# Kernel tuning notes

Hardware: AMD Instinct MI355X
Metric: run time of the kernel (lower is better)

The kernel has to match this reference:

```python
import jax, jax.numpy as jnp
import numpy as np

B, T, FEATS, HEAD = 2, 2048, 2048, 16
DIM_HEAD = FEATS // HEAD
EPS = float(jnp.finfo(jnp.float32).eps)  # torch nn.RMSNorm default eps=None -> dtype eps


def _rms_norm(u, g):
    # u: [..., d]; torch RMSNorm: u / sqrt(mean(u^2) + eps) * g
    return u * jax.lax.rsqrt(jnp.mean(u * u, axis=-1, keepdims=True) + EPS) * g


def setup_inputs() -> dict:
    key = jax.random.key(0)
    kx, kw = jax.random.split(key)
    x = jax.random.normal(kx, (B, T, FEATS), dtype=jnp.float32)
    W = jax.random.normal(kw, (FEATS, FEATS), dtype=jnp.float32) / np.sqrt(FEATS)
    g1 = jnp.ones((DIM_HEAD,), dtype=jnp.float32)
    g2 = jnp.ones((DIM_HEAD,), dtype=jnp.float32)
    g3 = jnp.ones((DIM_HEAD,), dtype=jnp.float32)
    return {"x": x, "W": W, "g1": g1, "g2": g2, "g3": g3}


def reference(x, W, g1, g2, g3):
    Bb, Tt, C = x.shape
    sqrt_d = jnp.asarray(DIM_HEAD ** 0.5, dtype=x.dtype)
    # tied QKV projection: torch Linear -> x @ W.T ; then split heads -> [B,H,T,D]
    w = (x @ W.T).reshape(Bb, Tt, HEAD, DIM_HEAD).transpose(0, 2, 1, 3)
    q = _rms_norm(w, g1)
    k = _rms_norm(w, g2)
    v = _rms_norm(w, g3)
    att = jnp.einsum("bhid,bhjd->bhij", q, k) / sqrt_d  # [B,H,T,T]
    # symmetric row + column softmax
    score = jax.nn.softmax(att, axis=-1) + jax.nn.softmax(att, axis=-2)
    y = jnp.einsum("bhij,bhjd->bihd", score, v).reshape(Bb, Tt, C)
    # F.linear(y, W.t()) == y @ W  (tied-weight reprojection)
    return y @ W
```

## Files before the change

### kernel.cpp

```cpp
#include <hip/hip_runtime.h>
#include <stdint.h>

#define T_SEQ 2048
#define B_SZ 2
#define N_HEAD 16
#define D_HEAD 128
#define C_DIM 2048
#define M_ROWS (B_SZ*T_SEQ)
#define N_BH (B_SZ*N_HEAD)

typedef _Float16 f16;
typedef f16 f16x8 __attribute__((ext_vector_type(8)));
typedef f16 f16x4 __attribute__((ext_vector_type(4)));
typedef float f32x4 __attribute__((ext_vector_type(4)));

#define MFMA_F16(a,b,c) __builtin_amdgcn_mfma_f32_16x16x32_f16(a,b,c,0,0,0)

#define BAR_LGKM() do { asm volatile("s_waitcnt lgkmcnt(0)" ::: "memory"); \
                        __builtin_amdgcn_s_barrier(); } while (0)
#define BAR_ALL()  do { asm volatile("s_waitcnt vmcnt(0) lgkmcnt(0)" ::: "memory"); \
                        __builtin_amdgcn_s_barrier(); } while (0)

__device__ __forceinline__ float fexp2(float x) {
#if __has_builtin(__builtin_amdgcn_exp2f)
  return __builtin_amdgcn_exp2f(x);
#else
  float r; asm("v_exp_f32 %0, %1" : "=v"(r) : "v"(x)); return r;
#endif
}

__device__ __forceinline__ void gl_lds16(const void* g, void* l) {
  __builtin_amdgcn_global_load_lds(
      (const __attribute__((address_space(1))) unsigned int*)g,
      (__attribute__((address_space(3))) unsigned int*)l, 16, 0, 0);
}

#define MB_SCALE 0.12752924444069595f
#define RMS_EPS  1.1920928955078125e-07f

__global__ void k_prep(const float* __restrict__ W, const float* __restrict__ x,
                       f16* __restrict__ Wb, f16* __restrict__ Wtb,
                       f16* __restrict__ xb) {
  __shared__ float tile[64][65];
  const int lin = blockIdx.x;
  const int t = threadIdx.x;
  if (lin < 1024) {
    const int bx = (lin & 31) * 64;
    const int by = (lin >> 5) * 64;
    const int tc = t & 63, tr4 = t >> 6;
    for (int rr = tr4; rr < 64; rr += 4) {
      float v = W[(size_t)(by + rr) * C_DIM + bx + tc];
      tile[rr][tc] = v;
      Wb[(size_t)(by + rr) * C_DIM + bx + tc] = (f16)v;
    }
    __syncthreads();
    for (int rr = tr4; rr < 64; rr += 4) {
      Wtb[(size_t)(bx + rr) * C_DIM + by + tc] = (f16)tile[tc][rr];
    }
  } else {
    int i = (lin - 1024) * 256 + t;
    const int stride = 2048 * 256;
    const int n4 = (M_ROWS * C_DIM) / 4;
    for (; i < n4; i += stride) {
      f32x4 v = ((const f32x4*)x)[i];
      f16x4 o; o[0]=(f16)v[0]; o[1]=(f16)v[1]; o[2]=(f16)v[2]; o[3]=(f16)v[3];
      ((f16x4*)xb)[i] = o;
    }
  }
}

template<typename OT>
__global__ __launch_bounds__(256, 2)
void k_gemm_bt(const f16* __restrict__ A, const f16* __restrict__ Bm,
               OT* __restrict__ C, int Nd, int Kd) {
  __shared__ __align__(16) f16 As[2][128 * 64];
  __shared__ __align__(16) f16 Bs[2][128 * 64];
  const int tid = threadIdx.x;
  const int lane = tid & 63, wid = tid >> 6;
  const int lr = lane & 15, lkg = lane >> 4;
  const int wr = wid >> 1, wc = wid & 1;
  const int tm = blockIdx.y * 128, tn = blockIdx.x * 128;

  f32x4 acc[4][4];
#pragma unroll
  for (int i = 0; i < 4; ++i)
#pragma unroll
    for (int j = 0; j < 4; ++j) acc[i][j] = (f32x4){0.f, 0.f, 0.f, 0.f};

  const int nkt = Kd >> 6;

  auto stage = [&](int buf, int kt) {
    const int k0 = kt << 6;
    for (int s = 0; s < 4; ++s) {
      const int r0 = (wid * 4 + s) * 8;
      const int r = r0 + (lane >> 3);
      const int lg = ((lane & 7) ^ (r & 7)) << 3;
      gl_lds16(A + (size_t)(tm + r) * Kd + k0 + lg, &As[buf][r0 * 64]);
      gl_lds16(Bm + (size_t)(tn + r) * Kd + k0 + lg, &Bs[buf][r0 * 64]);
    }
  };

  stage(0, 0);
  int cur = 0;
  for (int kt = 0; kt < nkt; ++kt) {
    __syncthreads();
    if (kt + 1 < nkt) stage(cur ^ 1, kt + 1);
#pragma unroll
    for (int kk = 0; kk < 2; ++kk) {
      f16x8 a[4], b[4];
#pragma unroll
      for (int i = 0; i < 4; ++i) {
        const int ra = wr * 64 + i * 16 + lr;
        const int ga = ((kk * 4 + lkg) ^ (ra & 7)) << 3;
        a[i] = *(const f16x8*)&As[cur][ra * 64 + ga];
        const int rb = wc * 64 + i * 16 + lr;
        const int gb = ((kk * 4 + lkg) ^ (rb & 7)) << 3;
        b[i] = *(const f16x8*)&Bs[cur][rb * 64 + gb];
      }
#pragma unroll
      for (int i = 0; i < 4; ++i)
#pragma unroll
        for (int j = 0; j < 4; ++j) acc[i][j] = MFMA_F16(a[i], b[j], acc[i][j]);
    }
    cur ^= 1;
  }
#pragma unroll
  for (int i = 0; i < 4; ++i) {
    const int row0 = tm + wr * 64 + i * 16 + lkg * 4;
#pragma unroll
    for (int j = 0; j < 4; ++j) {
      const int col = tn + wc * 64 + j * 16 + lr;
#pragma unroll
      for (int r = 0; r < 4; ++r)
        C[(size_t)(row0 + r) * Nd + col] = (OT)acc[i][j][r];
    }
  }
}

__global__ __launch_bounds__(256, 2)
void k_gemm_qkv(const f16* __restrict__ A, const f16* __restrict__ Bm,
                const float* __restrict__ g1, const float* __restrict__ g2,
                f16* __restrict__ nb, f16* __restrict__ mb,
                f16* __restrict__ nT) {
  __shared__ __align__(16) char smem[70656];
  f16 (*As)[128 * 64] = (f16(*)[128 * 64])smem;
  f16 (*Bs)[128 * 64] = (f16(*)[128 * 64])(smem + 32768);
  f16* Cs = (f16*)smem;
  float* sc = (float*)(smem + 69632);

  const int tid = threadIdx.x;
  const int lane = tid & 63, wid = tid >> 6;
  const int lr = lane & 15, lkg = lane >> 4;
  const int wr = wid >> 1, wc = wid & 1;
  const int tm = blockIdx.y * 128;
  const int hh = blockIdx.x;
  const int tn = hh * 128;

  f32x4 acc[4][4];
#pragma unroll
  for (int i = 0; i < 4; ++i)
#pragma unroll
    for (int j = 0; j < 4; ++j) acc[i][j] = (f32x4){0.f, 0.f, 0.f, 0.f};

  auto stage = [&](int buf, int kt) {
    const int k0 = kt << 6;
    for (int s = 0; s < 4; ++s) {
      const int r0 = (wid * 4 + s) * 8;
      const int r = r0 + (lane >> 3);
      const int lg = ((lane & 7) ^ (r & 7)) << 3;
      gl_lds16(A + (size_t)(tm + r) * C_DIM + k0 + lg, &As[buf][r0 * 64]);
      gl_lds16(Bm + (size_t)(tn + r) * C_DIM + k0 + lg, &Bs[buf][r0 * 64]);
    }
  };

  stage(0, 0);
  int cur = 0;
  for (int kt = 0; kt < 32; ++kt) {
    __syncthreads();
    if (kt + 1 < 32) stage(cur ^ 1, kt + 1);
#pragma unroll
    for (int kk = 0; kk < 2; ++kk) {
      f16x8 a[4], b[4];
#pragma unroll
      for (int i = 0; i < 4; ++i) {
        const int ra = wr * 64 + i * 16 + lr;
        const int ga = ((kk * 4 + lkg) ^ (ra & 7)) << 3;
        a[i] = *(const f16x8*)&As[cur][ra * 64 + ga];
        const int rb = wc * 64 + i * 16 + lr;
        const int gb = ((kk * 4 + lkg) ^ (rb & 7)) << 3;
        b[i] = *(const f16x8*)&Bs[cur][rb * 64 + gb];
      }
#pragma unroll
      for (int i = 0; i < 4; ++i)
#pragma unroll
        for (int j = 0; j < 4; ++j) acc[i][j] = MFMA_F16(a[i], b[j], acc[i][j]);
    }
    cur ^= 1;
  }
  __syncthreads();

#pragma unroll
  for (int i = 0; i < 4; ++i)
#pragma unroll
    for (int j = 0; j < 4; ++j)
#pragma unroll
      for (int r = 0; r < 4; ++r)
        Cs[(wr * 64 + i * 16 + lkg * 4 + r) * 136 + wc * 64 + j * 16 + lr] =
            (f16)acc[i][j][r];
  __syncthreads();

  const int row = tid >> 1, dh = tid & 1;
  f16x8 v[8];
  float ss = 0.f;
#pragma unroll
  for (int c = 0; c < 8; ++c) {
    v[c] = *(const f16x8*)&Cs[row * 136 + dh * 64 + c * 8];
#pragma unroll
    for (int e = 0; e < 8; ++e) { float f = (float)v[c][e]; ss += f * f; }
  }
  ss += __shfl_xor(ss, 1);
  const float scale = rsqrtf(ss * (1.f / 128.f) + RMS_EPS);
  if (dh == 0) sc[row] = scale;

  const int grow = tm + row;
  const int b = grow >> 11, ts = grow & (T_SEQ - 1);
  const size_t nbase =
      ((size_t)((b * N_HEAD + hh) * T_SEQ + ts)) * 128 + dh * 64;
#pragma unroll
  for (int c = 0; c < 8; ++c) {
    const int d0 = dh * 64 + c * 8;
    f16x8 n8, m8;
#pragma unroll
    for (int e = 0; e < 8; ++e) {
      const float nf = (float)v[c][e] * scale;
      n8[e] = (f16)nf;
      m8[e] = (f16)(nf * g1[d0 + e] * g2[d0 + e] * MB_SCALE);
    }
    *(f16x8*)&nb[nbase + c * 8] = n8;
    *(f16x8*)&mb[nbase + c * 8] = m8;
  }
  __syncthreads();

  const int dcol = tid >> 1, th = tid & 1;
  const size_t tbase =
      ((size_t)((b * N_HEAD + hh) * 128 + dcol)) * T_SEQ + (tm & (T_SEQ - 1)) +
      th * 64;
#pragma unroll
  for (int rr = 0; rr < 8; ++rr) {
    f16x8 o;
#pragma unroll
    for (int e = 0; e < 8; ++e) {
      const int trow = th * 64 + rr * 8 + e;
      o[e] = (f16)((float)Cs[trow * 136 + dcol] * sc[trow]);
    }
    *(f16x8*)&nT[tbase + rr * 8] = o;
  }
}

__global__ __launch_bounds__(256, 2)
void k_stats(const f16* __restrict__ mIn, const f16* __restrict__ nIn,
             float* __restrict__ alpha) {
  __shared__ __align__(16) f16 Ns[2][128 * 128];
  __shared__ float red[256];
  const int tid = threadIdx.x, lane = tid & 63, wid = tid >> 6;
  const int lr = lane & 15, lkg = lane >> 4;
  const int wr = wid >> 1, wc = wid & 1;
  const int lin = blockIdx.x + (blockIdx.y << 4);
  const int swz = ((lin & 7) << 6) + (lin >> 3);
  const int it = swz & 15, bh = swz >> 4;
  const f16* mp = mIn + (size_t)bh * T_SEQ * 128;
  const f16* np = nIn + (size_t)bh * T_SEQ * 128;

  f16x8 msr[4][4];
#pragma unroll
  for (int i = 0; i < 4; ++i)
#pragma unroll
    for (int kk = 0; kk < 4; ++kk)
      msr[i][kk] = *(const f16x8*)&mp[(size_t)(it * 128 + wr * 64 + i * 16 + lr) * 128 +
                                      (kk * 4 + lkg) * 8];

  auto stageN = [&](int buf, int jt) {
#pragma unroll
    for (int s = 0; s < 8; ++s) {
      const int r0 = (wid * 8 + s) * 4;
      const int r = r0 + (lane >> 4);
      const int lg = ((lane & 15) ^ (r & 7)) << 3;
      gl_lds16(np + (size_t)(jt * 128 + r) * 128 + lg, &Ns[buf][r0 * 128]);
    }
  };

  float srun[16];
#pragma unroll
  for (int q = 0; q < 16; ++q) srun[q] = 0.f;

  stageN(0, 0);
  BAR_ALL();
  int cur = 0;
  for (int jt = 0; jt < 16; ++jt) {
    if (jt < 15) stageN(cur ^ 1, jt + 1);
    f32x4 acc[4][4];
#pragma unroll
    for (int i = 0; i < 4; ++i)
#pragma unroll
      for (int j = 0; j < 4; ++j) acc[i][j] = (f32x4){0.f, 0.f, 0.f, 0.f};
#pragma unroll
    for (int kk = 0; kk < 4; ++kk) {
      f16x8 b[4];
#pragma unroll
      for (int j = 0; j < 4; ++j) {
        const int rb = wc * 64 + j * 16 + lr;
        const int gb = ((kk * 4 + lkg) ^ (rb & 7)) << 3;
        b[j] = *(const f16x8*)&Ns[cur][rb * 128 + gb];
      }
#pragma unroll
      for (int i = 0; i < 4; ++i)
#pragma unroll
        for (int j = 0; j < 4; ++j)
          acc[i][j] = MFMA_F16(msr[i][kk], b[j], acc[i][j]);
    }
#pragma unroll
    for (int i = 0; i < 4; ++i)
#pragma unroll
      for (int r = 0; r < 4; ++r) {
        float s = fexp2(acc[i][0][r]) + fexp2(acc[i][1][r]) +
                  fexp2(acc[i][2][r]) + fexp2(acc[i][3][r]);
        srun[i * 4 + r] += s;
      }
    BAR_ALL();
    cur ^= 1;
  }
#pragma unroll
  for (int q = 0; q < 16; ++q) {
    float v = srun[q];
    v += __shfl_xor(v, 1); v += __shfl_xor(v, 2);
    v += __shfl_xor(v, 4); v += __shfl_xor(v, 8);
    srun[q] = v;
  }
  if (lr == 0) {
#pragma unroll
    for (int q = 0; q < 16; ++q) {
      const int row = wr * 64 + (q >> 2) * 16 + lkg * 4 + (q & 3);
      red[row * 2 + wc] = srun[q];
    }
  }
  __syncthreads();
  if (tid < 128) {
    const float s = red[tid * 2] + red[tid * 2 + 1];
    alpha[(size_t)bh * T_SEQ + it * 128 + tid] = 1.f / s;
  }
}

__global__ __launch_bounds__(256, 2)
void k_apply(const f16* __restrict__ mIn, const f16* __restrict__ nIn,
             const f16* __restrict__ nTIn, const float* __restrict__ alpha,
             const float* __restrict__ g3, f16* __restrict__ yb) {
  __shared__ __align__(16) f16 Ns[2][64 * 128];
  __shared__ __align__(16) f16 Nts[2][128 * 64];
  __shared__ __align__(16) f16 Ps[128 * 64];
  const int tid = threadIdx.x, lane = tid & 63, wid = tid >> 6;
  const int lr = lane & 15, lkg = lane >> 4;
  const int wj = wid >> 1;
  const int wi = wid & 1;
  const int lin = blockIdx.x + (blockIdx.y << 4);
  const int swz = ((lin & 7) << 6) + (lin >> 3);
  const int it = swz & 15, bh = swz >> 4;
  const int b = bh >> 4, hh = bh & 15;
  const f16* mp = mIn + (size_t)bh * T_SEQ * 128;
  const f16* np = nIn + (size_t)bh * T_SEQ * 128;
  const f16* ntp = nTIn + (size_t)bh * 128 * T_SEQ;
  const float* al = alpha + (size_t)bh * T_SEQ;

  f16x8 msr[4][4];
#pragma unroll
  for (int ii = 0; ii < 4; ++ii)
#pragma unroll
    for (int kk = 0; kk < 4; ++kk)
      msr[ii][kk] = *(const f16x8*)&mp[(size_t)(it * 128 + wi * 64 + ii * 16 + lr) * 128 +
                                       (kk * 4 + lkg) * 8];

  auto stageN = [&](int buf, int jt) {
#pragma unroll
    for (int s = 0; s < 4; ++s) {
      const int r0 = (wid * 4 + s) * 4;
      const int r = r0 + (lane >> 4);
      const int lg = ((lane & 15) ^ (r & 7)) << 3;
      gl_lds16(np + (size_t)(jt * 64 + r) * 128 + lg, &Ns[buf][r0 * 128]);
    }
  };
  auto stageNT = [&](int buf, int jt) {
#pragma unroll
    for (int s = 0; s < 4; ++s) {
      const int r0 = (wid * 4 + s) * 8;
      const int r = r0 + (lane >> 3);
      const int lg = ((lane & 7) ^ (r & 7)) << 3;
      gl_lds16(ntp + (size_t)r * T_SEQ + jt * 64 + lg, &Nts[buf][r0 * 64]);
    }
  };

  float ai[4];
#pragma unroll
  for (int ii = 0; ii < 4; ++ii) ai[ii] = al[it * 128 + wi * 64 + ii * 16 + lr];

  f32x4 yacc[4][4];
#pragma unroll
  for (int i = 0; i < 4; ++i)
#pragma unroll
    for (int j = 0; j < 4; ++j) yacc[i][j] = (f32x4){0.f, 0.f, 0.f, 0.f};

  stageN(0, 0);
  stageNT(0, 0);
  BAR_ALL();
  int cur = 0;
  for (int jt = 0; jt < 32; ++jt) {
    float aj[8];
#pragma unroll
    for (int jj = 0; jj < 2; ++jj)
#pragma unroll
      for (int r = 0; r < 4; ++r)
        aj[jj * 4 + r] = al[jt * 64 + wj * 32 + jj * 16 + lkg * 4 + r];
    if (jt < 31) { stageN(cur ^ 1, jt + 1); stageNT(cur ^ 1, jt + 1); }

    f32x4 acc[2][4];
#pragma unroll
    for (int i = 0; i < 2; ++i)
#pragma unroll
      for (int j = 0; j < 4; ++j) acc[i][j] = (f32x4){0.f, 0.f, 0.f, 0.f};
#pragma unroll
    for (int kk = 0; kk < 4; ++kk) {
      f16x8 a[2];
#pragma unroll
      for (int jj = 0; jj < 2; ++jj) {
        const int jrow = wj * 32 + jj * 16 + lr;
        a[jj] = *(const f16x8*)&Ns[cur][jrow * 128 + (((kk * 4 + lkg) ^ (jrow & 7)) << 3)];
      }
#pragma unroll
      for (int jj = 0; jj < 2; ++jj)
#pragma unroll
        for (int ii = 0; ii < 4; ++ii)
          acc[jj][ii] = MFMA_F16(a[jj], msr[ii][kk], acc[jj][ii]);
    }

#pragma unroll
    for (int jj = 0; jj < 2; ++jj)
#pragma unroll
      for (int ii = 0; ii < 4; ++ii) {
        f16x4 o;
#pragma unroll
        for (int r = 0; r < 4; ++r) {
          const float p = fexp2(acc[jj][ii][r]) * (ai[ii] + aj[jj * 4 + r]);
          o[r] = (f16)p;
        }
        const int il = wi * 64 + ii * 16 + lr;
        const int jl = wj * 32 + jj * 16 + lkg * 4;
        *(f16x4*)&Ps[il * 64 + (((jl >> 3) ^ (il & 7)) << 3) + (jl & 7)] = o;
      }
    BAR_LGKM();

#pragma unroll
    for (int kk = 0; kk < 2; ++kk) {
      f16x8 a[4], bfr[4];
#pragma unroll
      for (int dd = 0; dd < 4; ++dd) {
        const int drow = wj * 64 + dd * 16 + lr;
        a[dd] = *(const f16x8*)&Nts[cur][drow * 64 + (((kk * 4 + lkg) ^ (drow & 7)) << 3)];
      }
#pragma unroll
      for (int ii = 0; ii < 4; ++ii) {
        const int irow = wi * 64 + ii * 16 + lr;
        bfr[ii] = *(const f16x8*)&Ps[irow * 64 + (((kk * 4 + lkg) ^ (irow & 7)) << 3)];
      }
#pragma unroll
      for (int dd = 0; dd < 4; ++dd)
#pragma unroll
        for (int ii = 0; ii < 4; ++ii)
          yacc[dd][ii] = MFMA_F16(a[dd], bfr[ii], yacc[dd][ii]);
    }
    BAR_ALL();
    cur ^= 1;
  }

#pragma unroll
  for (int dd = 0; dd < 4; ++dd) {
    const int d0 = wj * 64 + dd * 16 + lkg * 4;
    float g3v[4];
#pragma unroll
    for (int r = 0; r < 4; ++r) g3v[r] = g3[d0 + r];
#pragma unroll
    for (int ii = 0; ii < 4; ++ii) {
      const int icol = wi * 64 + ii * 16 + lr;
      const size_t base =
          ((size_t)(b * T_SEQ + it * 128 + icol)) * C_DIM + hh * 128 + d0;
      f16x4 o;
#pragma unroll
      for (int r = 0; r < 4; ++r) o[r] = (f16)(yacc[dd][ii][r] * g3v[r]);
      *(f16x4*)&yb[base] = o;
    }
  }
}

extern "C" void kernel_launch(void* const* d_in, const int* in_sizes, int n_in,
                              void* d_out, int out_size, void* d_ws,
                              size_t ws_size, hipStream_t stream) {
  const float* x = (const float*)d_in[0];
  const float* W = (const float*)d_in[1];
  const float* g1 = (const float*)d_in[2];
  const float* g2 = (const float*)d_in[3];
  const float* g3 = (const float*)d_in[4];
  float* out = (float*)d_out;
  char* ws = (char*)d_ws;

  f16* xb   = (f16*)(ws);
  f16* Wb   = (f16*)(ws + 16777216);
  f16* Wtb  = (f16*)(ws + 25165824);
  f16* nb   = (f16*)(ws + 50331648);
  f16* mb   = (f16*)(ws + 67108864);
  f16* nT   = (f16*)(ws + 83886080);
  f16* yb   = (f16*)(ws + 100663296);
  float* alpha = (float*)(ws + 117440512);

  k_prep<<<dim3(3072), 256, 0, stream>>>(W, x, Wb, Wtb, xb);
  k_gemm_qkv<<<dim3(16, 32), 256, 0, stream>>>(xb, Wb, g1, g2, nb, mb, nT);
  k_stats<<<dim3(16, 32), 256, 0, stream>>>(mb, nb, alpha);
  k_apply<<<dim3(16, 32), 256, 0, stream>>>(mb, nb, nT, alpha, g3, yb);
  k_gemm_bt<float><<<dim3(16, 32), 256, 0, stream>>>(yb, Wtb, out, C_DIM, C_DIM);
}
```

Baseline: 224.5 us.

## Keep P tile in registers via lane shuffles instead of LDS round-trip in k_apply

Each warp now owns 32 query rows and the full 64-column key tile and all 128 head dims, so the probability tile P produced by the first MFMA can feed the second MFMA directly. P is packed to fp16 pairs and rearranged across lanes with __shfl rather than written to and re-read from shared memory. This removes the Ps LDS buffer and the mid-loop barrier. In exchange, each warp reads the full Ns and Nts tiles from LDS (more LDS read traffic) and adds many cross-lane shuffles.

```diff
diff --git a/kernel.cpp b/kernel.cpp
--- a/kernel.cpp
+++ b/kernel.cpp
@@ -16,8 +16,6 @@
 
 #define MFMA_F16(a,b,c) __builtin_amdgcn_mfma_f32_16x16x32_f16(a,b,c,0,0,0)
 
-#define BAR_LGKM() do { asm volatile("s_waitcnt lgkmcnt(0)" ::: "memory"); \
-                        __builtin_amdgcn_s_barrier(); } while (0)
 #define BAR_ALL()  do { asm volatile("s_waitcnt vmcnt(0) lgkmcnt(0)" ::: "memory"); \
                         __builtin_amdgcn_s_barrier(); } while (0)
 
@@ -25,8 +23,14 @@
 #if __has_builtin(__builtin_amdgcn_exp2f)
   return __builtin_amdgcn_exp2f(x);
 #else
-  float r; asm("v_exp_f32 %0, %1" : "=v"(r) : "v"(x)); return r;
+  return exp2f(x);
 #endif
+}
+
+__device__ __forceinline__ uint32_t pkh(float a, float b) {
+  uint16_t ua = __builtin_bit_cast(uint16_t, (f16)a);
+  uint16_t ub = __builtin_bit_cast(uint16_t, (f16)b);
+  return (uint32_t)ua | ((uint32_t)ub << 16);
 }
 
 __device__ __forceinline__ void gl_lds16(const void* g, void* l) {
@@ -356,11 +360,9 @@
              const float* __restrict__ g3, f16* __restrict__ yb) {
   __shared__ __align__(16) f16 Ns[2][64 * 128];
   __shared__ __align__(16) f16 Nts[2][128 * 64];
-  __shared__ __align__(16) f16 Ps[128 * 64];
   const int tid = threadIdx.x, lane = tid & 63, wid = tid >> 6;
   const int lr = lane & 15, lkg = lane >> 4;
-  const int wj = wid >> 1;
-  const int wi = wid & 1;
+  const int w = wid;
   const int lin = blockIdx.x + (blockIdx.y << 4);
   const int swz = ((lin & 7) << 6) + (lin >> 3);
   const int it = swz & 15, bh = swz >> 4;
@@ -370,12 +372,12 @@
   const f16* ntp = nTIn + (size_t)bh * 128 * T_SEQ;
   const float* al = alpha + (size_t)bh * T_SEQ;
 
-  f16x8 msr[4][4];
-#pragma unroll
-  for (int ii = 0; ii < 4; ++ii)
+  f16x8 msr[2][4];
+#pragma unroll
+  for (int ii = 0; ii < 2; ++ii)
 #pragma unroll
     for (int kk = 0; kk < 4; ++kk)
-      msr[ii][kk] = *(const f16x8*)&mp[(size_t)(it * 128 + wi * 64 + ii * 16 + lr) * 128 +
+      msr[ii][kk] = *(const f16x8*)&mp[(size_t)(it * 128 + w * 32 + ii * 16 + lr) * 128 +
                                        (kk * 4 + lkg) * 8];
 
   auto stageN = [&](int buf, int jt) {
@@ -397,97 +399,115 @@
     }
   };
 
-  float ai[4];
-#pragma unroll
-  for (int ii = 0; ii < 4; ++ii) ai[ii] = al[it * 128 + wi * 64 + ii * 16 + lr];
-
-  f32x4 yacc[4][4];
-#pragma unroll
-  for (int i = 0; i < 4; ++i)
-#pragma unroll
-    for (int j = 0; j < 4; ++j) yacc[i][j] = (f32x4){0.f, 0.f, 0.f, 0.f};
+  float ai[2];
+#pragma unroll
+  for (int ii = 0; ii < 2; ++ii)
+    ai[ii] = al[it * 128 + w * 32 + ii * 16 + lr];
+
+  f32x4 yacc[8][2];
+#pragma unroll
+  for (int i = 0; i < 8; ++i)
+#pragma unroll
+    for (int j = 0; j < 2; ++j) yacc[i][j] = (f32x4){0.f, 0.f, 0.f, 0.f};
+
+  const int s0 = lr | ((lane & 16) << 1);
+  const int s1 = s0 + 16;
+  const bool hi = (lane & 32) != 0;
 
   stageN(0, 0);
   stageNT(0, 0);
   BAR_ALL();
   int cur = 0;
   for (int jt = 0; jt < 32; ++jt) {
-    float aj[8];
-#pragma unroll
-    for (int jj = 0; jj < 2; ++jj)
+    float aj[16];
+#pragma unroll
+    for (int jj = 0; jj < 4; ++jj)
 #pragma unroll
       for (int r = 0; r < 4; ++r)
-        aj[jj * 4 + r] = al[jt * 64 + wj * 32 + jj * 16 + lkg * 4 + r];
+        aj[jj * 4 + r] = al[jt * 64 + jj * 16 + lkg * 4 + r];
     if (jt < 31) { stageN(cur ^ 1, jt + 1); stageNT(cur ^ 1, jt + 1); }
 
-    f32x4 acc[2][4];
-#pragma unroll
-    for (int i = 0; i < 2; ++i)
-#pragma unroll
-      for (int j = 0; j < 4; ++j) acc[i][j] = (f32x4){0.f, 0.f, 0.f, 0.f};
+    f32x4 acc[4][2];
+#pragma unroll
+    for (int i = 0; i < 4; ++i)
+#pragma unroll
+      for (int j = 0; j < 2; ++j) acc[i][j] = (f32x4){0.f, 0.f, 0.f, 0.f};
 #pragma unroll
     for (int kk = 0; kk < 4; ++kk) {
-      f16x8 a[2];
-#pragma unroll
-      for (int jj = 0; jj < 2; ++jj) {
-        const int jrow = wj * 32 + jj * 16 + lr;
-        a[jj] = *(const f16x8*)&Ns[cur][jrow * 128 + (((kk * 4 + lkg) ^ (jrow & 7)) << 3)];
-      }
-#pragma unroll
-      for (int jj = 0; jj < 2; ++jj)
-#pragma unroll
-        for (int ii = 0; ii < 4; ++ii)
-          acc[jj][ii] = MFMA_F16(a[jj], msr[ii][kk], acc[jj][ii]);
-    }
-
-#pragma unroll
-    for (int jj = 0; jj < 2; ++jj)
-#pragma unroll
-      for (int ii = 0; ii < 4; ++ii) {
-        f16x4 o;
-#pragma unroll
-        for (int r = 0; r < 4; ++r) {
-          const float p = fexp2(acc[jj][ii][r]) * (ai[ii] + aj[jj * 4 + r]);
-          o[r] = (f16)p;
-        }
-        const int il = wi * 64 + ii * 16 + lr;
-        const int jl = wj * 32 + jj * 16 + lkg * 4;
-        *(f16x4*)&Ps[il * 64 + (((jl >> 3) ^ (il & 7)) << 3) + (jl & 7)] = o;
-      }
-    BAR_LGKM();
+      f16x8 aN[4];
+#pragma unroll
+      for (int jj = 0; jj < 4; ++jj) {
+        const int jrow = jj * 16 + lr;
+        aN[jj] = *(const f16x8*)&Ns[cur][jrow * 128 + (((kk * 4 + lkg) ^ (jrow & 7)) << 3)];
+      }
+#pragma unroll
+      for (int jj = 0; jj < 4; ++jj)
+#pragma unroll
+        for (int ii = 0; ii < 2; ++ii)
+          acc[jj][ii] = MFMA_F16(aN[jj], msr[ii][kk], acc[jj][ii]);
+    }
+
+    uint32_t pk[4][2][2];
+#pragma unroll
+    for (int jj = 0; jj < 4; ++jj)
+#pragma unroll
+      for (int ii = 0; ii < 2; ++ii) {
+        float p0 = fexp2(acc[jj][ii][0]) * (ai[ii] + aj[jj * 4 + 0]);
+        float p1 = fexp2(acc[jj][ii][1]) * (ai[ii] + aj[jj * 4 + 1]);
+        float p2 = fexp2(acc[jj][ii][2]) * (ai[ii] + aj[jj * 4 + 2]);
+        float p3 = fexp2(acc[jj][ii][3]) * (ai[ii] + aj[jj * 4 + 3]);
+        pk[jj][ii][0] = pkh(p0, p1);
+        pk[jj][ii][1] = pkh(p2, p3);
+      }
+
+    f16x8 bf[2][2];
+#pragma unroll
+    for (int kk = 0; kk < 2; ++kk)
+#pragma unroll
+      for (int ii = 0; ii < 2; ++ii) {
+        uint32_t a0 = (uint32_t)__shfl((int)pk[kk * 2 + 0][ii][0], s0);
+        uint32_t a1 = (uint32_t)__shfl((int)pk[kk * 2 + 0][ii][1], s0);
+        uint32_t a2 = (uint32_t)__shfl((int)pk[kk * 2 + 0][ii][0], s1);
+        uint32_t a3 = (uint32_t)__shfl((int)pk[kk * 2 + 0][ii][1], s1);
+        uint32_t b0 = (uint32_t)__shfl((int)pk[kk * 2 + 1][ii][0], s0);
+        uint32_t b1 = (uint32_t)__shfl((int)pk[kk * 2 + 1][ii][1], s0);
+        uint32_t b2 = (uint32_t)__shfl((int)pk[kk * 2 + 1][ii][0], s1);
+        uint32_t b3 = (uint32_t)__shfl((int)pk[kk * 2 + 1][ii][1], s1);
+        union { uint32_t wds[4]; f16x8 v; } u;
+        u.wds[0] = hi ? b0 : a0;
+        u.wds[1] = hi ? b1 : a1;
+        u.wds[2] = hi ? b2 : a2;
+        u.wds[3] = hi ? b3 : a3;
+        bf[kk][ii] = u.v;
+      }
 
 #pragma unroll
     for (int kk = 0; kk < 2; ++kk) {
-      f16x8 a[4], bfr[4];
-#pragma unroll
-      for (int dd = 0; dd < 4; ++dd) {
-        const int drow = wj * 64 + dd * 16 + lr;
-        a[dd] = *(const f16x8*)&Nts[cur][drow * 64 + (((kk * 4 + lkg) ^ (drow & 7)) << 3)];
-      }
-#pragma unroll
-      for (int ii = 0; ii < 4; ++ii) {
-        const int irow = wi * 64 + ii * 16 + lr;
-        bfr[ii] = *(const f16x8*)&Ps[irow * 64 + (((kk * 4 + lkg) ^ (irow & 7)) << 3)];
-      }
-#pragma unroll
-      for (int dd = 0; dd < 4; ++dd)
-#pragma unroll
-        for (int ii = 0; ii < 4; ++ii)
-          yacc[dd][ii] = MFMA_F16(a[dd], bfr[ii], yacc[dd][ii]);
+      f16x8 aT[8];
+#pragma unroll
+      for (int dd = 0; dd < 8; ++dd) {
+        const int drow = dd * 16 + lr;
+        aT[dd] = *(const f16x8*)&Nts[cur][drow * 64 + (((kk * 4 + lkg) ^ (drow & 7)) << 3)];
+      }
+#pragma unroll
+      for (int dd = 0; dd < 8; ++dd)
+#pragma unroll
+        for (int ii = 0; ii < 2; ++ii)
+          yacc[dd][ii] = MFMA_F16(aT[dd], bf[kk][ii], yacc[dd][ii]);
     }
     BAR_ALL();
     cur ^= 1;
   }
 
 #pragma unroll
-  for (int dd = 0; dd < 4; ++dd) {
-    const int d0 = wj * 64 + dd * 16 + lkg * 4;
+  for (int dd = 0; dd < 8; ++dd) {
+    const int d0 = dd * 16 + lkg * 4;
     float g3v[4];
 #pragma unroll
     for (int r = 0; r < 4; ++r) g3v[r] = g3[d0 + r];
 #pragma unroll
-    for (int ii = 0; ii < 4; ++ii) {
-      const int icol = wi * 64 + ii * 16 + lr;
+    for (int ii = 0; ii < 2; ++ii) {
+      const int icol = w * 32 + ii * 16 + lr;
       const size_t base =
           ((size_t)(b * T_SEQ + it * 128 + icol)) * C_DIM + hh * 128 + d0;
       f16x4 o;
```

Result: slower. 242.1 us (+7.8%).
